# Performance work log

Hardware: AMD Instinct MI355X
Metric: run time of the kernel (lower is better)

The kernel has to match this reference:

```python
import jax, jax.numpy as jnp
import numpy as np

N = 50000      # nodes
E = 1200000    # edges
G = 256        # graphs in batch
H = 64         # hidden_dim
F_IN = 5       # input_dim
L = 3          # num deep GCN layers
EPS_BN = 1e-5
EPS_MSG = 1e-7

def setup_inputs() -> dict:
    key = jax.random.key(0)
    ks = jax.random.split(key, 12)
    r = lambda i, shp, s=0.1: jax.random.normal(ks[i], shp, jnp.float32) * s
    return {
        "x": jax.random.normal(ks[0], (N, F_IN), jnp.float32),
        "edge_index": jax.random.randint(ks[1], (2, E), 0, N),
        "batch_idx": jnp.sort(jax.random.randint(ks[2], (N,), 0, G)),
        "conv1_W": r(3, (F_IN, H)), "conv1_b": jnp.zeros((H,), jnp.float32),
        "bn1_g": jnp.ones((H,), jnp.float32), "bn1_b": jnp.zeros((H,), jnp.float32),
        "ln_g": jnp.ones((L, H), jnp.float32), "ln_b": jnp.zeros((L, H), jnp.float32),
        "prelu_a": jnp.full((L, H), 0.25, jnp.float32),
        "gen_t": jnp.ones((L,), jnp.float32),
        "mlp_W1": r(4, (L, H, 2 * H)), "mlp_b1": jnp.zeros((L, 2 * H), jnp.float32),
        "mlp_bn_g": jnp.ones((L, 2 * H), jnp.float32), "mlp_bn_b": jnp.zeros((L, 2 * H), jnp.float32),
        "mlp_W2": r(5, (L, 2 * H, H)), "mlp_b2": jnp.zeros((L, H), jnp.float32),
        "lin1_W": r(6, ((L + 1) * H * 2, 2 * H)), "lin1_b": jnp.zeros((2 * H,), jnp.float32),
        "lin2_W": r(7, (2 * H, H)), "lin2_b": jnp.zeros((H,), jnp.float32),
        "out_W": r(8, (H, 1)), "out_b": jnp.zeros((1,), jnp.float32),
    }

def _layernorm(x, g, b):
    mu = jnp.mean(x, axis=-1, keepdims=True)
    var = jnp.mean(jnp.square(x - mu), axis=-1, keepdims=True)
    return (x - mu) * jax.lax.rsqrt(var + EPS_BN) * g + b

def _prelu(x, a):
    return jnp.where(x >= 0, x, a * x)

def _bn_eval(x, g, b):
    # eval-mode BatchNorm with running_mean=0, running_var=1
    return x * (g / jnp.sqrt(1.0 + EPS_BN)) + b

def reference(x, edge_index, batch_idx, conv1_W, conv1_b, bn1_g, bn1_b,
              ln_g, ln_b, prelu_a, gen_t, mlp_W1, mlp_b1, mlp_bn_g, mlp_bn_b,
              mlp_W2, mlp_b2, lin1_W, lin1_b, lin2_W, lin2_b, out_W, out_b):
    n = x.shape[0]
    src, dst = edge_index[0], edge_index[1]

    # ---- GCNConv (with self loops, symmetric normalization) ----
    loops = jnp.arange(n)
    row = jnp.concatenate([src, loops])  # [E+N]
    col = jnp.concatenate([dst, loops])
    h = x @ conv1_W
    deg = jax.ops.segment_sum(jnp.ones_like(col, jnp.float32), col, num_segments=n)
    dinv = jnp.where(deg > 0, deg ** -0.5, 0.0)
    norm = dinv[row] * dinv[col]
    h = jax.ops.segment_sum(h[row] * norm[:, None], col, num_segments=n) + conv1_b
    h = _bn_eval(h, bn1_g, bn1_b)
    h = jax.nn.relu(h)

    xs = [h]
    # ---- DeepGCNLayer (res+) x L, GENConv with softmax aggregation ----
    for i in range(ln_g.shape[0]):
        u = _layernorm(h, ln_g[i], ln_b[i])
        u = _prelu(u, prelu_a[i])
        msg = jax.nn.relu(u[src]) + EPS_MSG            # [E, H]
        sc = msg * gen_t[i]
        m = jax.ops.segment_max(sc, dst, num_segments=n)
        e = jnp.exp(sc - m[dst])
        s = jax.ops.segment_sum(e, dst, num_segments=n)
        alpha = e / s[dst]                             # segment-wise softmax per channel
        agg = jax.ops.segment_sum(msg * alpha, dst, num_segments=n) + u  # root add
        z = agg @ mlp_W1[i] + mlp_b1[i]
        z = _bn_eval(z, mlp_bn_g[i], mlp_bn_b[i])
        z = jax.nn.relu(z)
        z = z @ mlp_W2[i] + mlp_b2[i]
        h = h + z                                      # res+
        xs.append(h)

    # ---- JumpingKnowledge cat + global mean/max pool ----
    xc = jnp.concatenate(xs, axis=1)                   # [N, 4H]
    cnt = jax.ops.segment_sum(jnp.ones((n,), jnp.float32), batch_idx, num_segments=G)
    xmean = jax.ops.segment_sum(xc, batch_idx, num_segments=G) / jnp.maximum(cnt, 1.0)[:, None]
    xmax = jax.ops.segment_max(xc, batch_idx, num_segments=G)
    xmax = jnp.where(jnp.isfinite(xmax), xmax, 0.0)
    p = jnp.concatenate([xmean, xmax], axis=1)         # [G, 8H]

    # ---- readout MLP (dropout off in eval) ----
    p = jax.nn.relu(p @ lin1_W + lin1_b)
    p = jax.nn.relu(p @ lin2_W + lin2_b)
    return p @ out_W + out_b
```

## Files before the change

### kernel.cpp

```cpp
#include <hip/hip_runtime.h>
#include <math.h>

#define NND 50000
#define NE  1200000
#define NG  256
#define H   64
#define H2  128
#define H4  256
#define H8  512
#define FIN 5
#define EPS_BN 1e-5f
#define EPS_MSG 1e-7f
#define NB 196
#define TILES 196
#define TCAP 7168
#define EPB 4096
#define NB1 293
#define MRG (NB + 14)
#define ELLC 72
#define PC 8
#define MT 64

typedef _Float16 half8 __attribute__((ext_vector_type(8)));
typedef _Float16 half4 __attribute__((ext_vector_type(4)));
typedef float floatx4 __attribute__((ext_vector_type(4)));


__global__ void __launch_bounds__(256)
k_setup(const int* __restrict__ batch, int* tilecur, int* __restrict__ gstart,
        const float* __restrict__ x, float* __restrict__ xp,
        const float* __restrict__ W1, const float* __restrict__ W2,
        _Float16* __restrict__ w1f, _Float16* __restrict__ w2f,
        const int* __restrict__ ei, unsigned* __restrict__ tilebuf) {
    __shared__ int cnt[TILES];
    __shared__ int base[TILES];
    int b = blockIdx.x, t = threadIdx.x;
    if (b >= MRG) {
        int bb = b - MRG;
        for (int i = t; i < TILES; i += 256) cnt[i] = 0;
        __syncthreads();
        int e0 = bb * EPB;
#pragma unroll
        for (int r = 0; r < EPB / 256; r++) {
            int e = e0 + r * 256 + t;
            if (e < NE) atomicAdd(&cnt[ei[NE + e] >> 8], 1);
        }
        __syncthreads();
        for (int i = t; i < TILES; i += 256) {
            base[i] = atomicAdd(&tilecur[i], cnt[i]);
            cnt[i] = 0;
        }
        __syncthreads();
#pragma unroll
        for (int r = 0; r < EPB / 256; r++) {
            int e = e0 + r * 256 + t;
            if (e < NE) {
                int s = ei[e], d = ei[NE + e];
                int tile = d >> 8;
                int pos = base[tile] + atomicAdd(&cnt[tile], 1);
                if (pos < TCAP)
                    tilebuf[(size_t)tile * TCAP + pos] = ((unsigned)s << 8) | (unsigned)(d & 255);
            }
        }
        return;
    }
    if (b < NB) {
        int n = b * 256 + t;
        if (n < NND) {
            float a0 = x[n * FIN + 0], a1 = x[n * FIN + 1], a2 = x[n * FIN + 2];
            float a3 = x[n * FIN + 3], a4 = x[n * FIN + 4];
            *(float4*)&xp[n * 8] = make_float4(a0, a1, a2, a3);
            *(float4*)&xp[n * 8 + 4] = make_float4(a4, 0.f, 0.f, 0.f);
        }
        return;
    }
    if (b == NB || b == NB + 1) {
        int g = (b - NB) * 256 + t;
        if (g > NG) return;
        int lo = 0, hi = NND;
        while (lo < hi) { int mid = (lo + hi) >> 1; if (batch[mid] < g) lo = mid + 1; else hi = mid; }
        gstart[g] = lo;
        return;
    }
    int tt = (b - NB - 2) * 256 + t;
    if (tt >= 3 * 16 * 64) return;
    int lane = tt & 63, fr = (tt >> 6) & 15, l = tt >> 10;
    {
        int jt = fr >> 1, kf = fr & 1;
        int j = jt * 16 + (lane & 15);
        int k0 = kf * 32 + (lane >> 4) * 8;
#pragma unroll
        for (int i = 0; i < 8; i++)
            w1f[(((size_t)l * 16 + jt * 2 + kf) * 64 + lane) * 8 + i] =
                (_Float16)W1[(size_t)l * H * H2 + (k0 + i) * H2 + j];
    }
    {
        int ct = fr >> 2, k2f = fr & 3;
        int c = ct * 16 + (lane & 15);
        int k0 = k2f * 32 + (lane >> 4) * 8;
#pragma unroll
        for (int i = 0; i < 8; i++)
            w2f[(((size_t)l * 16 + ct * 4 + k2f) * 64 + lane) * 8 + i] =
                (_Float16)W2[(size_t)l * H2 * H + (k0 + i) * H + c];
    }
}


__global__ void __launch_bounds__(256)
k_bin2(const int* __restrict__ tilecur, const unsigned* __restrict__ tilebuf,
       unsigned short* __restrict__ ell, int* __restrict__ deg, float* __restrict__ xp) {
    __shared__ unsigned short ell_l[256 * ELLC];
    __shared__ int cnt[256];
    int tile = blockIdx.x, t = threadIdx.x;
    cnt[t] = 0;
    __syncthreads();
    int n = min(tilecur[tile], TCAP);
    for (int i = t; i < n; i += 256) {
        unsigned v = __builtin_nontemporal_load(&tilebuf[(size_t)tile * TCAP + i]);
        int dl = v & 255u;
        int slot = atomicAdd(&cnt[dl], 1);
        if (slot < ELLC) ell_l[dl * ELLC + slot] = (unsigned short)(v >> 8);
    }
    __syncthreads();
    const unsigned* s32 = (const unsigned*)ell_l;
    unsigned* d32 = (unsigned*)(ell + (size_t)tile * 256 * ELLC);
    for (int i = t; i < 256 * ELLC / 2; i += 256) d32[i] = s32[i];
    int d = tile * 256 + t;
    if (d < NND) {
        deg[d] = min(cnt[t], ELLC);
        xp[(size_t)d * 8 + 5] = rsqrtf((float)cnt[t] + 1.0f);
    }
}


__global__ void k_gcn(const int* __restrict__ deg, const unsigned short* __restrict__ ell,
                      const float* __restrict__ xp,
                      const float* __restrict__ W,
                      const float* __restrict__ cb, const float* __restrict__ bg,
                      const float* __restrict__ bb,
                      const float* __restrict__ lg, const float* __restrict__ lb,
                      const float* __restrict__ pa,
                      _Float16* __restrict__ xcH, _Float16* __restrict__ u_h) {
    int tid = blockIdx.x * blockDim.x + threadIdx.x;
    int d = tid >> 4;
    int r = threadIdx.x & 15;
    if (d >= NND) return;
    int dg = deg[d];
    size_t base = (size_t)d * ELLC;
    float xw0 = 0.f, xw1 = 0.f, xw2 = 0.f, xw3 = 0.f, xw4 = 0.f;
    for (int i = r; i < dg; i += 16) {
        int s = (int)__builtin_nontemporal_load(&ell[base + i]);
        float4 a = *(const float4*)&xp[s * 8];
        float2 a45 = *(const float2*)&xp[s * 8 + 4];
        float dv = a45.y;
        xw0 += a.x * dv; xw1 += a.y * dv; xw2 += a.z * dv;
        xw3 += a.w * dv; xw4 += a45.x * dv;
    }
#pragma unroll
    for (int off = 1; off <= 8; off <<= 1) {
        xw0 += __shfl_xor(xw0, off, 64);
        xw1 += __shfl_xor(xw1, off, 64);
        xw2 += __shfl_xor(xw2, off, 64);
        xw3 += __shfl_xor(xw3, off, 64);
        xw4 += __shfl_xor(xw4, off, 64);
    }
    float4 xa = *(const float4*)&xp[d * 8];
    float2 xa45 = *(const float2*)&xp[d * 8 + 4];
    float dd = xa45.y;
    xw0 += dd * xa.x; xw1 += dd * xa.y; xw2 += dd * xa.z;
    xw3 += dd * xa.w; xw4 += dd * xa45.x;
    float bns = rsqrtf(1.f + EPS_BN);
    float x0[4];
    float sum = 0.f, sq = 0.f;
#pragma unroll
    for (int j = 0; j < 4; j++) {
        int c = 4 * r + j;
        float s_ = xw0 * W[c] + xw1 * W[H + c] + xw2 * W[2 * H + c]
                 + xw3 * W[3 * H + c] + xw4 * W[4 * H + c];
        float v = s_ * dd + cb[c];
        v = v * (bg[c] * bns) + bb[c];
        v = fmaxf(v, 0.f);
        x0[j] = v;
        sum += v; sq += v * v;
    }
    {
        half4 xh = {(_Float16)x0[0], (_Float16)x0[1], (_Float16)x0[2], (_Float16)x0[3]};
        *(half4*)&xcH[(size_t)d * H4 + 4 * r] = xh;
    }
#pragma unroll
    for (int off = 1; off <= 8; off <<= 1) {
        sum += __shfl_xor(sum, off, 64);
        sq  += __shfl_xor(sq,  off, 64);
    }
    float mu  = sum * (1.f / H);
    float var = sq * (1.f / H) - mu * mu;
    float rs = rsqrtf(var + EPS_BN);
    half4 yh;
#pragma unroll
    for (int j = 0; j < 4; j++) {
        int c = 4 * r + j;
        float y = (x0[j] - mu) * rs * lg[c] + lb[c];
        y = (y >= 0.f) ? y : pa[c] * y;
        yh[j] = (_Float16)y;
    }
    *(half4*)&u_h[(size_t)d * H + 4 * r] = yh;
}


__global__ void k_gen(const int* __restrict__ deg, const unsigned short* __restrict__ ell,
                      const _Float16* __restrict__ u_h,
                      const float* __restrict__ tptr, int li, _Float16* __restrict__ ua_h) {
    int d = (blockIdx.x * blockDim.x + threadIdx.x) >> 6;
    int lane = threadIdx.x & 63;
    if (d >= NND) return;
    int q = lane & 15, eg = lane >> 4;
    float t = tptr[li];
    int dg = deg[d];
    size_t base = (size_t)d * ELLC;
    half4 us = *(const half4*)&u_h[(size_t)d * H + 4 * q];
    float4 s4 = {0.f, 0.f, 0.f, 0.f}, n4 = {0.f, 0.f, 0.f, 0.f};
    for (int i0 = 0; i0 < dg; i0 += 64) {
        int idx = i0 + lane;
        int csrv = (idx < dg) ? (int)__builtin_nontemporal_load(&ell[base + idx]) : 0;
        int chunk = min(64, dg - i0);
        for (int j = 0; j < chunk; j += 32) {
            half4 uv[8]; bool ok[8];
#pragma unroll
            for (int b2 = 0; b2 < 8; b2++) {
                int e_rel = j + 4 * b2 + eg;
                int s = __shfl(csrv, e_rel, 64);
                ok[b2] = (e_rel < chunk);
                uv[b2] = (half4){0, 0, 0, 0};
                if (ok[b2]) uv[b2] = *(const half4*)&u_h[(size_t)s * H + 4 * q];
            }
#pragma unroll
            for (int b2 = 0; b2 < 8; b2++) {
                if (ok[b2]) {
                    float m0 = fmaxf((float)uv[b2][0], 0.f) + EPS_MSG;
                    float m1 = fmaxf((float)uv[b2][1], 0.f) + EPS_MSG;
                    float m2 = fmaxf((float)uv[b2][2], 0.f) + EPS_MSG;
                    float m3 = fmaxf((float)uv[b2][3], 0.f) + EPS_MSG;
                    float e0 = __expf(m0 * t - 8.f);
                    float e1 = __expf(m1 * t - 8.f);
                    float e2 = __expf(m2 * t - 8.f);
                    float e3 = __expf(m3 * t - 8.f);
                    s4.x += e0; s4.y += e1; s4.z += e2; s4.w += e3;
                    n4.x += m0 * e0; n4.y += m1 * e1; n4.z += m2 * e2; n4.w += m3 * e3;
                }
            }
        }
    }
#pragma unroll
    for (int off = 16; off <= 32; off <<= 1) {
        s4.x += __shfl_xor(s4.x, off, 64); s4.y += __shfl_xor(s4.y, off, 64);
        s4.z += __shfl_xor(s4.z, off, 64); s4.w += __shfl_xor(s4.w, off, 64);
        n4.x += __shfl_xor(n4.x, off, 64); n4.y += __shfl_xor(n4.y, off, 64);
        n4.z += __shfl_xor(n4.z, off, 64); n4.w += __shfl_xor(n4.w, off, 64);
    }
    if (eg == 0) {
        float o0 = (float)us[0] + ((s4.x > 0.f) ? n4.x / s4.x : 0.f);
        float o1 = (float)us[1] + ((s4.y > 0.f) ? n4.y / s4.y : 0.f);
        float o2 = (float)us[2] + ((s4.z > 0.f) ? n4.z / s4.z : 0.f);
        float o3 = (float)us[3] + ((s4.w > 0.f) ? n4.w / s4.w : 0.f);
        half4 oh = {(_Float16)o0, (_Float16)o1, (_Float16)o2, (_Float16)o3};
        *(half4*)&ua_h[(size_t)d * H + 4 * q] = oh;
    }
}


__global__ void __launch_bounds__(256)
k_mlp(const _Float16* __restrict__ ua_h,
      const _Float16* __restrict__ w1f, const _Float16* __restrict__ w2f,
      const float* __restrict__ b1,
      const float* __restrict__ bng, const float* __restrict__ bnb,
      const float* __restrict__ b2,
      _Float16* __restrict__ xcH, int slice,
      const float* __restrict__ lg, const float* __restrict__ lb,
      const float* __restrict__ pa, _Float16* __restrict__ u_h, int do_ln) {
    __shared__ _Float16 a2[4][4][64][8];
    int t = threadIdx.x;
    int w = t >> 6, l = t & 63;
    int nb = blockIdx.x * MT;
    int c_in = l & 15, quad = l >> 4;
    bool wvalid = (nb + 16 * w) < NND;

    half8 af0 = {0,0,0,0,0,0,0,0}, af1 = af0;
    {
        int node = nb + 16 * w + c_in;
        if (node < NND) {
            af0 = *(const half8*)&ua_h[(size_t)node * H + quad * 8];
            af1 = *(const half8*)&ua_h[(size_t)node * H + 32 + quad * 8];
        }
    }

    floatx4 acc[8];
#pragma unroll
    for (int jt = 0; jt < 8; jt++) acc[jt] = (floatx4){0.f, 0.f, 0.f, 0.f};
#pragma unroll
    for (int jt = 0; jt < 8; jt++) {
        half8 bf0 = *(const half8*)&w1f[((size_t)(jt * 2 + 0) * 64 + l) * 8];
        half8 bf1 = *(const half8*)&w1f[((size_t)(jt * 2 + 1) * 64 + l) * 8];
        acc[jt] = __builtin_amdgcn_mfma_f32_16x16x32_f16(af0, bf0, acc[jt], 0, 0, 0);
        acc[jt] = __builtin_amdgcn_mfma_f32_16x16x32_f16(af1, bf1, acc[jt], 0, 0, 0);
    }

    {
        float bns = rsqrtf(1.f + EPS_BN);
#pragma unroll
        for (int jt = 0; jt < 8; jt++) {
            int j = jt * 16 + c_in;
            float b1v = b1[j], bsv = bng[j] * bns, bbv = bnb[j];
            int kf2 = jt >> 1;
            int lp = 16 * ((2 * jt + (c_in >> 3)) & 3);
            int ii = c_in & 7;
#pragma unroll
            for (int reg = 0; reg < 4; reg++) {
                float z = fmaxf((acc[jt][reg] + b1v) * bsv + bbv, 0.f);
                a2[w][kf2][quad * 4 + reg + lp][ii] = (_Float16)z;
            }
        }
    }

    floatx4 acc2[4];
#pragma unroll
    for (int ct = 0; ct < 4; ct++) acc2[ct] = (floatx4){0.f, 0.f, 0.f, 0.f};
    half8 a2f[4];
#pragma unroll
    for (int k2f = 0; k2f < 4; k2f++) a2f[k2f] = *(half8*)&a2[w][k2f][l][0];
#pragma unroll
    for (int ct = 0; ct < 4; ct++) {
#pragma unroll
        for (int k2f = 0; k2f < 4; k2f++) {
            half8 bfr = *(const half8*)&w2f[((size_t)(ct * 4 + k2f) * 64 + l) * 8];
            acc2[ct] = __builtin_amdgcn_mfma_f32_16x16x32_f16(a2f[k2f], bfr, acc2[ct], 0, 0, 0);
        }
    }

    float vv[4][4];
#pragma unroll
    for (int ct = 0; ct < 4; ct++) {
        int c = ct * 16 + c_in;
        float b2v = b2[c];
#pragma unroll
        for (int reg = 0; reg < 4; reg++) {
            int node = nb + 16 * w + quad * 4 + reg;
            float v = 0.f;
            if (wvalid) {
                v = (float)xcH[(size_t)node * H4 + slice * H + c] + acc2[ct][reg] + b2v;
                xcH[(size_t)node * H4 + (slice + 1) * H + c] = (_Float16)v;
            }
            vv[ct][reg] = v;
        }
    }
    if (do_ln) {
#pragma unroll
        for (int reg = 0; reg < 4; reg++) {
            float s = (vv[0][reg] + vv[1][reg]) + (vv[2][reg] + vv[3][reg]);
            float q = (vv[0][reg] * vv[0][reg] + vv[1][reg] * vv[1][reg]) +
                      (vv[2][reg] * vv[2][reg] + vv[3][reg] * vv[3][reg]);
#pragma unroll
            for (int off = 1; off <= 8; off <<= 1) {
                s += __shfl_xor(s, off, 64);
                q += __shfl_xor(q, off, 64);
            }
            float mu = s * (1.f / H);
            float var = q * (1.f / H) - mu * mu;
            float rs = rsqrtf(var + EPS_BN);
            int node = nb + 16 * w + quad * 4 + reg;
#pragma unroll
            for (int ct = 0; ct < 4; ct++) {
                int c = ct * 16 + c_in;
                float y = (vv[ct][reg] - mu) * rs * lg[c] + lb[c];
                y = (y >= 0.f) ? y : pa[c] * y;
                if (wvalid) u_h[(size_t)node * H + c] = (_Float16)y;
            }
        }
    }
}


__global__ void __launch_bounds__(256)
k_pool1(const _Float16* __restrict__ xcH, const int* __restrict__ gstart,
        float* __restrict__ psum_p, float* __restrict__ pmax_p) {
    __shared__ float4 ssum[256];
    __shared__ float4 smax[256];
    int b = blockIdx.x;
    int g = b >> 3, k = b & (PC - 1);
    int t = threadIdx.x;
    int start = gstart[g], end = gstart[g + 1];
    int len = end - start;
    int c0 = start + (len * k) / PC;
    int c1 = start + (len * (k + 1)) / PC;
    int q = t & 63, sub = t >> 6;
    float4 sum = {0.f, 0.f, 0.f, 0.f};
    float4 mx = {-INFINITY, -INFINITY, -INFINITY, -INFINITY};
    for (int n = c0 + sub; n < c1; n += 4) {
        half4 vh = __builtin_nontemporal_load((const half4*)&xcH[(size_t)n * H4 + 4 * q]);
        float v0 = (float)vh[0], v1 = (float)vh[1], v2 = (float)vh[2], v3 = (float)vh[3];
        sum.x += v0; sum.y += v1; sum.z += v2; sum.w += v3;
        mx.x = fmaxf(mx.x, v0); mx.y = fmaxf(mx.y, v1);
        mx.z = fmaxf(mx.z, v2); mx.w = fmaxf(mx.w, v3);
    }
    ssum[t] = sum; smax[t] = mx;
    __syncthreads();
    if (t < 64) {
        float4 s0 = ssum[t], s1 = ssum[t + 64], s2 = ssum[t + 128], s3 = ssum[t + 192];
        float4 m0 = smax[t], m1 = smax[t + 64], m2 = smax[t + 128], m3 = smax[t + 192];
        float4 S, M;
        S.x = (s0.x + s1.x) + (s2.x + s3.x);
        S.y = (s0.y + s1.y) + (s2.y + s3.y);
        S.z = (s0.z + s1.z) + (s2.z + s3.z);
        S.w = (s0.w + s1.w) + (s2.w + s3.w);
        M.x = fmaxf(fmaxf(m0.x, m1.x), fmaxf(m2.x, m3.x));
        M.y = fmaxf(fmaxf(m0.y, m1.y), fmaxf(m2.y, m3.y));
        M.z = fmaxf(fmaxf(m0.z, m1.z), fmaxf(m2.z, m3.z));
        M.w = fmaxf(fmaxf(m0.w, m1.w), fmaxf(m2.w, m3.w));
        *(float4*)&psum_p[(size_t)b * H4 + 4 * q] = S;
        *(float4*)&pmax_p[(size_t)b * H4 + 4 * q] = M;
    }
}

__global__ void __launch_bounds__(256)
k_readout(const float* __restrict__ psum_p, const float* __restrict__ pmax_p,
          const int* __restrict__ gstart,
          const float* __restrict__ W1, const float* __restrict__ b1,
          const float* __restrict__ W2, const float* __restrict__ b2,
          const float* __restrict__ Wo, const float* __restrict__ bo,
          float* __restrict__ out) {
    __shared__ float p0_l[H8];
    __shared__ float p1part[2][H2];
    __shared__ float p1_l[H2];
    __shared__ float p2part[4][H];
    __shared__ float p2_l[H];
    int g = blockIdx.x;
    int t = threadIdx.x;

    {
        float s = 0.f, m = -INFINITY;
#pragma unroll
        for (int k = 0; k < PC; k++) {
            s += psum_p[(size_t)(g * PC + k) * H4 + t];
            m = fmaxf(m, pmax_p[(size_t)(g * PC + k) * H4 + t]);
        }
        int cnt = gstart[g + 1] - gstart[g];
        p0_l[t] = s / fmaxf((float)cnt, 1.f);
        p0_l[H4 + t] = (cnt > 0) ? m : 0.f;
    }
    __syncthreads();

    {
        int j = t & 127, h = t >> 7;
        float acc = 0.f;
        int k0 = h * 256;
        for (int k = 0; k < 256; k++) acc += p0_l[k0 + k] * W1[(k0 + k) * H2 + j];
        p1part[h][j] = acc;
    }
    __syncthreads();
    if (t < H2) p1_l[t] = fmaxf(p1part[0][t] + p1part[1][t] + b1[t], 0.f);
    __syncthreads();

    {
        int c = t & 63, h = t >> 6;
        float acc = 0.f;
        int k0 = h * 32;
        for (int k = 0; k < 32; k++) acc += p1_l[k0 + k] * W2[(k0 + k) * H + c];
        p2part[h][c] = acc;
    }
    __syncthreads();
    if (t < H) p2_l[t] = fmaxf(((p2part[0][t] + p2part[1][t]) + (p2part[2][t] + p2part[3][t])) + b2[t], 0.f);
    __syncthreads();

    if (t < 64) {
        float v = p2_l[t] * Wo[t];
#pragma unroll
        for (int off = 32; off >= 1; off >>= 1) v += __shfl_xor(v, off, 64);
        if (t == 0) out[g] = v + bo[0];
    }
}

extern "C" void kernel_launch(void* const* d_in, const int* in_sizes, int n_in,
                              void* d_out, int out_size, void* d_ws, size_t ws_size,
                              hipStream_t stream) {
    const float* x       = (const float*)d_in[0];
    const int*   ei      = (const int*)d_in[1];
    const int*   batch   = (const int*)d_in[2];
    const float* conv1_W = (const float*)d_in[3];
    const float* conv1_b = (const float*)d_in[4];
    const float* bn1_g   = (const float*)d_in[5];
    const float* bn1_b   = (const float*)d_in[6];
    const float* ln_g    = (const float*)d_in[7];
    const float* ln_b    = (const float*)d_in[8];
    const float* prelu_a = (const float*)d_in[9];
    const float* gen_t   = (const float*)d_in[10];
    const float* mlp_W1  = (const float*)d_in[11];
    const float* mlp_b1  = (const float*)d_in[12];
    const float* mlp_bng = (const float*)d_in[13];
    const float* mlp_bnb = (const float*)d_in[14];
    const float* mlp_W2  = (const float*)d_in[15];
    const float* mlp_b2  = (const float*)d_in[16];
    const float* lin1_W  = (const float*)d_in[17];
    const float* lin1_b  = (const float*)d_in[18];
    const float* lin2_W  = (const float*)d_in[19];
    const float* lin2_b  = (const float*)d_in[20];
    const float* out_W   = (const float*)d_in[21];
    const float* out_b   = (const float*)d_in[22];
    float* out = (float*)d_out;

    float* ws   = (float*)d_ws;
    _Float16* xcH = (_Float16*)ws;
    float* xp   = (float*)(xcH + (size_t)NND * H4);
    int* deg    = (int*)(xp + (size_t)NND * 8);
    int* gstart = deg + NND;
    int* tilecur = gstart + NG + 1;
    unsigned* tilebuf = (unsigned*)(tilecur + TILES);
    unsigned short* ell = (unsigned short*)(tilebuf + (size_t)TILES * TCAP);
    uintptr_t wb = (uintptr_t)(ell + (size_t)TILES * 256 * ELLC);
    wb = (wb + 15) & ~(uintptr_t)15;
    _Float16* w1f = (_Float16*)wb;
    _Float16* w2f = w1f + 3 * 8192;
    _Float16* u_h  = w2f + 3 * 8192;
    _Float16* ua_h = u_h + (size_t)NND * H;
    uintptr_t pb = (uintptr_t)(ua_h + (size_t)NND * H);
    pb = (pb + 15) & ~(uintptr_t)15;
    float* psum_p = (float*)pb;
    float* pmax_p = psum_p + (size_t)NG * PC * H4;

    const int B = 256;
    const int gGCN = (NND * 16 + B - 1) / B;
    const int gNH  = (NND * H) / B;
    const int gMLP = (NND + MT - 1) / MT;

    hipMemsetAsync(tilecur, 0, TILES * sizeof(int), stream);
    k_setup<<<MRG + NB1, B, 0, stream>>>(batch, tilecur, gstart, x, xp,
                                         mlp_W1, mlp_W2, w1f, w2f, ei, tilebuf);
    k_bin2<<<TILES, B, 0, stream>>>(tilecur, tilebuf, ell, deg, xp);

    k_gcn<<<gGCN, B, 0, stream>>>(deg, ell, xp, conv1_W, conv1_b, bn1_g, bn1_b,
                                  ln_g, ln_b, prelu_a, xcH, u_h);

    for (int i = 0; i < 3; i++) {
        k_gen<<<gNH, B, 0, stream>>>(deg, ell, u_h, gen_t, i, ua_h);
        int do_ln = (i < 2) ? 1 : 0;
        k_mlp<<<gMLP, B, 0, stream>>>(ua_h,
                                      w1f + (size_t)i * 8192, w2f + (size_t)i * 8192,
                                      mlp_b1 + i * H2,
                                      mlp_bng + i * H2, mlp_bnb + i * H2,
                                      mlp_b2 + i * H,
                                      xcH, i,
                                      ln_g + (i + 1) * H, ln_b + (i + 1) * H,
                                      prelu_a + (i + 1) * H, u_h, do_ln);
    }

    k_pool1<<<NG * PC, B, 0, stream>>>(xcH, gstart, psum_p, pmax_p);
    k_readout<<<NG, B, 0, stream>>>(psum_p, pmax_p, gstart,
                                    lin1_W, lin1_b, lin2_W, lin2_b, out_W, out_b, out);
}
```

Measured before the change: 331.6 us.

## Fuse global mean/max pooling into GCN and MLP epilogues via atomics

Removes the separate pooling kernel that re-read the full concatenated fp16 feature buffer. Instead, the GCN and per-layer MLP kernels reduce their freshly computed outputs per graph inside each block and push partial sums and maxima to global accumulators. The sums use float atomicAdd and the maxima use atomicMax on an order-preserving unsigned mapping of the float. This saves a large memory pass and a kernel launch, in exchange for extra block syncs and per-graph loops in those epilogues, an added memset, and nondeterministic float summation order.

```diff
diff --git a/kernel.cpp b/kernel.cpp
--- a/kernel.cpp
+++ b/kernel.cpp
@@ -18,12 +18,16 @@
 #define NB1 293
 #define MRG (NB + 14)
 #define ELLC 72
-#define PC 8
 #define MT 64
 
 typedef _Float16 half8 __attribute__((ext_vector_type(8)));
 typedef _Float16 half4 __attribute__((ext_vector_type(4)));
 typedef float floatx4 __attribute__((ext_vector_type(4)));
+
+__device__ __forceinline__ unsigned fmap_max(float f) {
+    unsigned b = __float_as_uint(f);
+    return (b & 0x80000000u) ? ~b : (b | 0x80000000u);
+}
 
 
 __global__ void __launch_bounds__(256)
@@ -140,7 +144,11 @@
                       const float* __restrict__ bb,
                       const float* __restrict__ lg, const float* __restrict__ lb,
                       const float* __restrict__ pa,
-                      _Float16* __restrict__ xcH, _Float16* __restrict__ u_h) {
+                      _Float16* __restrict__ xcH, _Float16* __restrict__ u_h,
+                      const int* __restrict__ batch,
+                      float* __restrict__ psum, unsigned* __restrict__ pmax_u) {
+    __shared__ float ps[4][64];
+    __shared__ float pm[4][64];
     int tid = blockIdx.x * blockDim.x + threadIdx.x;
     int d = tid >> 4;
     int r = threadIdx.x & 15;
@@ -204,6 +212,41 @@
         yh[j] = (_Float16)y;
     }
     *(half4*)&u_h[(size_t)d * H + 4 * r] = yh;
+
+    int first = blockIdx.x * 16;
+    int gd = batch[d];
+    int g_lo = batch[first], g_hi = batch[first + 15];
+    int w = threadIdx.x >> 6;
+    for (int g = g_lo; g <= g_hi; ++g) {
+        bool m_ = (gd == g);
+        float s0 = m_ ? x0[0] : 0.f, s1 = m_ ? x0[1] : 0.f;
+        float s2 = m_ ? x0[2] : 0.f, s3 = m_ ? x0[3] : 0.f;
+        float m0 = m_ ? x0[0] : -INFINITY, m1 = m_ ? x0[1] : -INFINITY;
+        float m2 = m_ ? x0[2] : -INFINITY, m3 = m_ ? x0[3] : -INFINITY;
+#pragma unroll
+        for (int off = 16; off <= 32; off <<= 1) {
+            s0 += __shfl_xor(s0, off, 64); s1 += __shfl_xor(s1, off, 64);
+            s2 += __shfl_xor(s2, off, 64); s3 += __shfl_xor(s3, off, 64);
+            m0 = fmaxf(m0, __shfl_xor(m0, off, 64)); m1 = fmaxf(m1, __shfl_xor(m1, off, 64));
+            m2 = fmaxf(m2, __shfl_xor(m2, off, 64)); m3 = fmaxf(m3, __shfl_xor(m3, off, 64));
+        }
+        if ((threadIdx.x & 63) < 16) {
+            ps[w][4 * r + 0] = s0; ps[w][4 * r + 1] = s1;
+            ps[w][4 * r + 2] = s2; ps[w][4 * r + 3] = s3;
+            pm[w][4 * r + 0] = m0; pm[w][4 * r + 1] = m1;
+            pm[w][4 * r + 2] = m2; pm[w][4 * r + 3] = m3;
+        }
+        __syncthreads();
+        if (threadIdx.x < 64) {
+            float S = (ps[0][threadIdx.x] + ps[1][threadIdx.x]) +
+                      (ps[2][threadIdx.x] + ps[3][threadIdx.x]);
+            float M = fmaxf(fmaxf(pm[0][threadIdx.x], pm[1][threadIdx.x]),
+                            fmaxf(pm[2][threadIdx.x], pm[3][threadIdx.x]));
+            atomicAdd(&psum[(size_t)g * H4 + threadIdx.x], S);
+            atomicMax(&pmax_u[(size_t)g * H4 + threadIdx.x], fmap_max(M));
+        }
+        __syncthreads();
+    }
 }
 
 
@@ -276,8 +319,12 @@
       const float* __restrict__ b2,
       _Float16* __restrict__ xcH, int slice,
       const float* __restrict__ lg, const float* __restrict__ lb,
-      const float* __restrict__ pa, _Float16* __restrict__ u_h, int do_ln) {
+      const float* __restrict__ pa, _Float16* __restrict__ u_h, int do_ln,
+      const int* __restrict__ batch,
+      float* __restrict__ psum, unsigned* __restrict__ pmax_u) {
     __shared__ _Float16 a2[4][4][64][8];
+    __shared__ float pls[4][64];
+    __shared__ float plm[4][64];
     int t = threadIdx.x;
     int w = t >> 6, l = t & 63;
     int nb = blockIdx.x * MT;
@@ -376,52 +423,56 @@
             }
         }
     }
+
+    int gd_r[4];
+#pragma unroll
+    for (int reg = 0; reg < 4; reg++) {
+        int node = nb + 16 * w + quad * 4 + reg;
+        gd_r[reg] = (node < NND) ? batch[node] : -1;
+    }
+    int g_lo = batch[nb];
+    int g_hi = batch[min(nb + 63, NND - 1)];
+    int chbase = (slice + 1) * H;
+    for (int g = g_lo; g <= g_hi; ++g) {
+        float sc[4], mc[4];
+#pragma unroll
+        for (int ct = 0; ct < 4; ct++) {
+            float s_ = 0.f, m_ = -INFINITY;
+#pragma unroll
+            for (int reg = 0; reg < 4; reg++) {
+                if (gd_r[reg] == g) { s_ += vv[ct][reg]; m_ = fmaxf(m_, vv[ct][reg]); }
+            }
+            sc[ct] = s_; mc[ct] = m_;
+        }
+#pragma unroll
+        for (int off = 16; off <= 32; off <<= 1) {
+#pragma unroll
+            for (int ct = 0; ct < 4; ct++) {
+                sc[ct] += __shfl_xor(sc[ct], off, 64);
+                mc[ct] = fmaxf(mc[ct], __shfl_xor(mc[ct], off, 64));
+            }
+        }
+        if (l < 16) {
+#pragma unroll
+            for (int ct = 0; ct < 4; ct++) {
+                pls[w][ct * 16 + l] = sc[ct];
+                plm[w][ct * 16 + l] = mc[ct];
+            }
+        }
+        __syncthreads();
+        if (t < 64) {
+            float S = (pls[0][t] + pls[1][t]) + (pls[2][t] + pls[3][t]);
+            float M = fmaxf(fmaxf(plm[0][t], plm[1][t]), fmaxf(plm[2][t], plm[3][t]));
+            atomicAdd(&psum[(size_t)g * H4 + chbase + t], S);
+            atomicMax(&pmax_u[(size_t)g * H4 + chbase + t], fmap_max(M));
+        }
+        __syncthreads();
+    }
 }
 
 
 __global__ void __launch_bounds__(256)
-k_pool1(const _Float16* __restrict__ xcH, const int* __restrict__ gstart,
-        float* __restrict__ psum_p, float* __restrict__ pmax_p) {
-    __shared__ float4 ssum[256];
-    __shared__ float4 smax[256];
-    int b = blockIdx.x;
-    int g = b >> 3, k = b & (PC - 1);
-    int t = threadIdx.x;
-    int start = gstart[g], end = gstart[g + 1];
-    int len = end - start;
-    int c0 = start + (len * k) / PC;
-    int c1 = start + (len * (k + 1)) / PC;
-    int q = t & 63, sub = t >> 6;
-    float4 sum = {0.f, 0.f, 0.f, 0.f};
-    float4 mx = {-INFINITY, -INFINITY, -INFINITY, -INFINITY};
-    for (int n = c0 + sub; n < c1; n += 4) {
-        half4 vh = __builtin_nontemporal_load((const half4*)&xcH[(size_t)n * H4 + 4 * q]);
-        float v0 = (float)vh[0], v1 = (float)vh[1], v2 = (float)vh[2], v3 = (float)vh[3];
-        sum.x += v0; sum.y += v1; sum.z += v2; sum.w += v3;
-        mx.x = fmaxf(mx.x, v0); mx.y = fmaxf(mx.y, v1);
-        mx.z = fmaxf(mx.z, v2); mx.w = fmaxf(mx.w, v3);
-    }
-    ssum[t] = sum; smax[t] = mx;
-    __syncthreads();
-    if (t < 64) {
-        float4 s0 = ssum[t], s1 = ssum[t + 64], s2 = ssum[t + 128], s3 = ssum[t + 192];
-        float4 m0 = smax[t], m1 = smax[t + 64], m2 = smax[t + 128], m3 = smax[t + 192];
-        float4 S, M;
-        S.x = (s0.x + s1.x) + (s2.x + s3.x);
-        S.y = (s0.y + s1.y) + (s2.y + s3.y);
-        S.z = (s0.z + s1.z) + (s2.z + s3.z);
-        S.w = (s0.w + s1.w) + (s2.w + s3.w);
-        M.x = fmaxf(fmaxf(m0.x, m1.x), fmaxf(m2.x, m3.x));
-        M.y = fmaxf(fmaxf(m0.y, m1.y), fmaxf(m2.y, m3.y));
-        M.z = fmaxf(fmaxf(m0.z, m1.z), fmaxf(m2.z, m3.z));
-        M.w = fmaxf(fmaxf(m0.w, m1.w), fmaxf(m2.w, m3.w));
-        *(float4*)&psum_p[(size_t)b * H4 + 4 * q] = S;
-        *(float4*)&pmax_p[(size_t)b * H4 + 4 * q] = M;
-    }
-}
-
-__global__ void __launch_bounds__(256)
-k_readout(const float* __restrict__ psum_p, const float* __restrict__ pmax_p,
+k_readout(const float* __restrict__ psum, const unsigned* __restrict__ pmax_u,
           const int* __restrict__ gstart,
           const float* __restrict__ W1, const float* __restrict__ b1,
           const float* __restrict__ W2, const float* __restrict__ b2,
@@ -436,13 +487,10 @@
     int t = threadIdx.x;
 
     {
-        float s = 0.f, m = -INFINITY;
-#pragma unroll
-        for (int k = 0; k < PC; k++) {
-            s += psum_p[(size_t)(g * PC + k) * H4 + t];
-            m = fmaxf(m, pmax_p[(size_t)(g * PC + k) * H4 + t]);
-        }
         int cnt = gstart[g + 1] - gstart[g];
+        float s = psum[(size_t)g * H4 + t];
+        unsigned u = pmax_u[(size_t)g * H4 + t];
+        float m = (u & 0x80000000u) ? __uint_as_float(u & 0x7FFFFFFFu) : __uint_as_float(~u);
         p0_l[t] = s / fmaxf((float)cnt, 1.f);
         p0_l[H4 + t] = (cnt > 0) ? m : 0.f;
     }
@@ -522,8 +570,8 @@
     _Float16* ua_h = u_h + (size_t)NND * H;
     uintptr_t pb = (uintptr_t)(ua_h + (size_t)NND * H);
     pb = (pb + 15) & ~(uintptr_t)15;
-    float* psum_p = (float*)pb;
-    float* pmax_p = psum_p + (size_t)NG * PC * H4;
+    float* psum = (float*)pb;
+    unsigned* pmax_u = (unsigned*)(psum + (size_t)NG * H4);
 
     const int B = 256;
     const int gGCN = (NND * 16 + B - 1) / B;
@@ -531,12 +579,14 @@
     const int gMLP = (NND + MT - 1) / MT;
 
     hipMemsetAsync(tilecur, 0, TILES * sizeof(int), stream);
+    hipMemsetAsync(psum, 0, (size_t)NG * H4 * (sizeof(float) + sizeof(unsigned)), stream);
     k_setup<<<MRG + NB1, B, 0, stream>>>(batch, tilecur, gstart, x, xp,
                                          mlp_W1, mlp_W2, w1f, w2f, ei, tilebuf);
     k_bin2<<<TILES, B, 0, stream>>>(tilecur, tilebuf, ell, deg, xp);
 
     k_gcn<<<gGCN, B, 0, stream>>>(deg, ell, xp, conv1_W, conv1_b, bn1_g, bn1_b,
-                                  ln_g, ln_b, prelu_a, xcH, u_h);
+                                  ln_g, ln_b, prelu_a, xcH, u_h,
+                                  batch, psum, pmax_u);
 
     for (int i = 0; i < 3; i++) {
         k_gen<<<gNH, B, 0, stream>>>(deg, ell, u_h, gen_t, i, ua_h);
@@ -548,10 +598,10 @@
                                       mlp_b2 + i * H,
                                       xcH, i,
                                       ln_g + (i + 1) * H, ln_b + (i + 1) * H,
-                                      prelu_a + (i + 1) * H, u_h, do_ln);
-    }
-
-    k_pool1<<<NG * PC, B, 0, stream>>>(xcH, gstart, psum_p, pmax_p);
-    k_readout<<<NG, B, 0, stream>>>(psum_p, pmax_p, gstart,
+                                      prelu_a + (i + 1) * H, u_h, do_ln,
+                                      batch, psum, pmax_u);
+    }
+
+    k_readout<<<NG, B, 0, stream>>>(psum, pmax_u, gstart,
                                     lin1_W, lin1_b, lin2_W, lin2_b, out_W, out_b, out);
 }
```

Result: no change. 332.8 us (+0.4%).
